# Kernel optimization log

Hardware: AMD Instinct MI355X
Metric: run time of the kernel (lower is better)

Reference implementation:

```python
import jax, jax.numpy as jnp
import numpy as np

B, N, ENC = 128, 196, 2048
DEC, ATT, EMB, V, T = 512, 512, 512, 10000, 21


def setup_inputs() -> dict:
    key = jax.random.key(0)
    ks = jax.random.split(key, 20)
    g = lambda k, shape, scale=0.02: jax.random.normal(k, shape, dtype=jnp.float32) * scale
    return {
        "features": jax.random.normal(ks[0], (B, N, ENC), dtype=jnp.float32),
        "captions": jax.random.randint(ks[1], (B, T), 0, V),
        "emb": g(ks[2], (V, EMB)),
        # attention (weights stored [in, out])
        "U_w": g(ks[3], (ENC, ATT)), "U_b": jnp.zeros((ATT,), jnp.float32),
        "W_w": g(ks[4], (DEC, ATT)), "W_b": jnp.zeros((ATT,), jnp.float32),
        "A_w": g(ks[5], (ATT, 1)),   "A_b": jnp.zeros((1,), jnp.float32),
        # init hidden state
        "ih_w": g(ks[6], (ENC, DEC)), "ih_b": jnp.zeros((DEC,), jnp.float32),
        "ic_w": g(ks[7], (ENC, DEC)), "ic_b": jnp.zeros((DEC,), jnp.float32),
        # LSTMCell, torch gate order (i, f, g, o); stored [in, 4*DEC]
        "lstm_Wih": g(ks[8], (EMB + ENC, 4 * DEC)),
        "lstm_Whh": g(ks[9], (DEC, 4 * DEC)),
        "lstm_bih": jnp.zeros((4 * DEC,), jnp.float32),
        "lstm_bhh": jnp.zeros((4 * DEC,), jnp.float32),
        # output projection
        "fcn_w": g(ks[10], (DEC, V)), "fcn_b": jnp.zeros((V,), jnp.float32),
    }


def reference(features, captions, emb, U_w, U_b, W_w, W_b, A_w, A_b,
              ih_w, ih_b, ic_w, ic_b,
              lstm_Wih, lstm_Whh, lstm_bih, lstm_bhh, fcn_w, fcn_b):
    # init hidden state from mean-pooled features
    mean_feat = features.mean(axis=1)                      # [B, ENC]
    h0 = mean_feat @ ih_w + ih_b                           # [B, DEC]
    c0 = mean_feat @ ic_w + ic_b

    # U(features) is constant across timesteps -> precompute
    u_hs = jnp.einsum('bne,ea->bna', features, U_w) + U_b  # [B, N, ATT]

    embeds = emb[captions[:, :T - 1]]                       # [B, S, EMB]
    embeds_t = jnp.swapaxes(embeds, 0, 1)                   # [S, B, EMB]

    def step(carry, emb_t):
        h, c = carry
        # Bahdanau attention
        w_ah = h @ W_w + W_b                                # [B, ATT]
        scores = (jnp.tanh(u_hs + w_ah[:, None, :]) @ A_w)[..., 0] + A_b[0]  # [B, N]
        alpha = jax.nn.softmax(scores, axis=1)
        context = jnp.einsum('bn,bne->be', alpha, features) # [B, ENC]
        # LSTMCell
        x = jnp.concatenate([emb_t, context], axis=1)       # [B, EMB+ENC]
        gates = x @ lstm_Wih + lstm_bih + h @ lstm_Whh + lstm_bhh
        i, f, g, o = jnp.split(gates, 4, axis=1)
        c = jax.nn.sigmoid(f) * c + jax.nn.sigmoid(i) * jnp.tanh(g)
        h = jax.nn.sigmoid(o) * jnp.tanh(c)
        out = h @ fcn_w + fcn_b                             # [B, V] (dropout = identity in eval)
        return (h, c), (out, alpha)

    (_, _), (preds_t, alphas_t) = jax.lax.scan(step, (h0, c0), embeds_t)
    preds = jnp.swapaxes(preds_t, 0, 1)                     # [B, S, V]
    alphas = jnp.swapaxes(alphas_t, 0, 1)                   # [B, S, N]
    return preds, alphas
```

## Files before the change

### kernel.cpp

```cpp
#include <hip/hip_runtime.h>
#include <cmath>

#define B_   128
#define N_   196
#define ENC_ 2048
#define DEC_ 512
#define ATT_ 512
#define EMB_ 512
#define V_   10000
#define TS_  20
#define HCAT_ 12672
#define HOUT_ 2560

typedef unsigned short u16;
typedef short s16x8 __attribute__((ext_vector_type(8)));
typedef float f32x4 __attribute__((ext_vector_type(4)));
typedef unsigned short u16x4 __attribute__((ext_vector_type(4)));

__device__ __forceinline__ float sigmoidf_(float x) { return 1.0f / (1.0f + expf(-x)); }

__device__ __forceinline__ float fast_tanh(float x) {
  float cx = fminf(fmaxf(x, -8.f), 8.f);
  float e = __expf(2.f * cx);
  return (e - 1.f) * __builtin_amdgcn_rcpf(e + 1.f);
}

__device__ __forceinline__ u16 f2bf(float x) {
  union { float f; unsigned u; } v; v.f = x;
  unsigned r = v.u + 0x7fff + ((v.u >> 16) & 1);
  return (u16)(r >> 16);
}
__device__ __forceinline__ float bf2f(u16 h) {
  union { float f; unsigned u; } v; v.u = ((unsigned)h) << 16; return v.f;
}

typedef const __attribute__((address_space(1))) void gas_t;
typedef __attribute__((address_space(3))) void las_t;
__device__ __forceinline__ void gld_lds16(const void* g, void* l) {
  __builtin_amdgcn_global_load_lds((gas_t*)g, (las_t*)l, 16, 0, 0);
}

__global__ __launch_bounds__(256, 2) void k_mfma(
    const u16* __restrict__ A, int lda,
    const u16* __restrict__ Bt, int ldb,
    const float* __restrict__ bias,
    float* __restrict__ C, u16* __restrict__ Cb, int ldc, int Nbound,
    float* __restrict__ C2, int csplit, int ldc2,
    int K, int atomic) {
  __shared__ __align__(16) u16 As[2][128 * 32];
  __shared__ __align__(16) u16 Bs[2][128 * 32];

  const int tid = threadIdx.x;
  const int bm = blockIdx.y * 128;
  const int bn = blockIdx.x * 128;
  const int kchunk = K / gridDim.z;
  const int k0 = blockIdx.z * kchunk;
  const int kend = k0 + kchunk;

  const int r0 = tid >> 2;
  const int kb = (tid & 3) * 8;
  const u16* ga0 = A + (size_t)(bm + r0) * lda + kb;
  const u16* ga1 = A + (size_t)(bm + 64 + r0) * lda + kb;
  const u16* gb0 = Bt + (size_t)(bn + r0) * ldb + kb;
  const u16* gb1 = Bt + (size_t)(bn + 64 + r0) * ldb + kb;

  const int w = tid >> 6;
  const int lane = tid & 63;
  const int wm = (w & 1) * 64;
  const int wn = (w >> 1) * 64;
  const int r16 = lane & 15;
  const int kq = lane >> 4;

  f32x4 acc[4][4] = {};

  auto STAGE = [&](int buf, int k) {
    gld_lds16(ga0 + k, &As[buf][tid * 8]);
    gld_lds16(ga1 + k, &As[buf][2048 + tid * 8]);
    gld_lds16(gb0 + k, &Bs[buf][tid * 8]);
    gld_lds16(gb1 + k, &Bs[buf][2048 + tid * 8]);
  };

  STAGE(0, k0);
  __syncthreads();
  int cur = 0;
  for (int k = k0; k < kend; k += 32) {
    if (k + 32 < kend) STAGE(cur ^ 1, k + 32);
    s16x8 af[4], bfr[4];
#pragma unroll
    for (int i = 0; i < 4; ++i)
      af[i] = *(const s16x8*)&As[cur][(wm + i * 16 + r16) * 32 + kq * 8];
#pragma unroll
    for (int i = 0; i < 4; ++i)
      bfr[i] = *(const s16x8*)&Bs[cur][(wn + i * 16 + r16) * 32 + kq * 8];
#pragma unroll
    for (int mi = 0; mi < 4; ++mi)
#pragma unroll
      for (int ni = 0; ni < 4; ++ni)
        acc[mi][ni] = __builtin_amdgcn_mfma_f32_16x16x32_bf16(af[mi], bfr[ni], acc[mi][ni], 0, 0, 0);
    __syncthreads();
    cur ^= 1;
  }

#pragma unroll
  for (int ni = 0; ni < 4; ++ni) {
    int col = bn + wn + ni * 16 + r16;
    if (col < Nbound) {
      float bv = bias ? bias[col] : 0.f;
#pragma unroll
      for (int mi = 0; mi < 4; ++mi) {
#pragma unroll
        for (int r = 0; r < 4; ++r) {
          int row = bm + wm + mi * 16 + kq * 4 + r;
          float v = acc[mi][ni][r] + bv;
          if (atomic)                     atomicAdd(&C[(size_t)row * ldc + col], v);
          else if (Cb)                    Cb[(size_t)row * ldc + col] = f2bf(v);
          else if (C2 && col >= csplit)   C2[(size_t)row * ldc2 + (col - csplit)] = v;
          else                            C[(size_t)row * ldc + col] = v;
        }
      }
    }
  }
}

__global__ __launch_bounds__(256) void k_wt(const float* __restrict__ in, int K, int N,
                                            u16* __restrict__ out, int ldo, int Nout) {
  __shared__ float s[32][33];
  int k0 = blockIdx.x * 32, n0 = blockIdx.y * 32;
  int tx = threadIdx.x & 31, ty = threadIdx.x >> 5;
#pragma unroll
  for (int i = 0; i < 4; ++i) {
    int k = k0 + ty + i * 8, n = n0 + tx;
    s[ty + i * 8][tx] = (n < N) ? in[(size_t)k * N + n] : 0.f;
  }
  __syncthreads();
#pragma unroll
  for (int i = 0; i < 4; ++i) {
    int n = n0 + ty + i * 8;
    if (n < Nout) out[(size_t)n * ldo + k0 + tx] = f2bf(s[tx][ty + i * 8]);
  }
}

__global__ __launch_bounds__(256) void k_hbias(const float* __restrict__ W_b,
                                               const float* __restrict__ bih,
                                               const float* __restrict__ bhh,
                                               const float* __restrict__ fcn_b,
                                               float* __restrict__ hbias) {
  int i = blockIdx.x * 256 + threadIdx.x;
  if (i >= HCAT_) return;
  float v;
  if (i < 512)        v = W_b[i];
  else if (i < 2560)  v = bih[i - 512] + bhh[i - 512];
  else if (i < 12560) v = fcn_b[i - 2560];
  else                v = 0.f;
  hbias[i] = v;
}

__global__ __launch_bounds__(256) void k_embed_all(const float* __restrict__ emb,
                                                   const int* __restrict__ captions,
                                                   u16* __restrict__ emb_all_bf) {
  int r = blockIdx.y;
  int t = r >> 7, b = r & 127;
  int k = blockIdx.x * 256 + threadIdx.x;
  int tok = captions[b * 21 + t];
  emb_all_bf[(size_t)r * EMB_ + k] = f2bf(emb[(size_t)tok * EMB_ + k]);
}

__global__ __launch_bounds__(256) void k_cvtmean(const float* __restrict__ f,
                                                 u16* __restrict__ feat_bf,
                                                 u16* __restrict__ mean_bf) {
  int b = blockIdx.y;
  int e = (blockIdx.x * 256 + threadIdx.x) * 4;
  const float* p = f + (size_t)b * N_ * ENC_ + e;
  u16* q = feat_bf + (size_t)b * N_ * ENC_ + e;
  float s0 = 0.f, s1 = 0.f, s2 = 0.f, s3 = 0.f;
#pragma unroll 2
  for (int n = 0; n < N_; ++n) {
    float4 v = *(const float4*)(p + (size_t)n * ENC_);
    s0 += v.x; s1 += v.y; s2 += v.z; s3 += v.w;
    u16x4 o; o.x = f2bf(v.x); o.y = f2bf(v.y); o.z = f2bf(v.z); o.w = f2bf(v.w);
    *(u16x4*)(q + (size_t)n * ENC_) = o;
  }
  const float inv = 1.0f / (float)N_;
  u16x4 m; m.x = f2bf(s0 * inv); m.y = f2bf(s1 * inv);
  m.z = f2bf(s2 * inv); m.w = f2bf(s3 * inv);
  *(u16x4*)(mean_bf + b * ENC_ + e) = m;
}

__global__ __launch_bounds__(256) void k_scores(const u16* __restrict__ u_hs,
                                                const float* __restrict__ w_ah, int ldw,
                                                const float* __restrict__ A_w,
                                                const float* __restrict__ A_b,
                                                float* __restrict__ scores) {
  int wave = threadIdx.x >> 6;
  int lane = threadIdx.x & 63;
  int bn = blockIdx.x * 4 + wave;
  int b = bn / N_;
  int a0 = lane * 8;
  const u16* up = u_hs + (size_t)bn * ATT_ + a0;
  const float* wp = w_ah + (size_t)b * ldw + a0;
  float s = 0.f;
#pragma unroll
  for (int j = 0; j < 2; ++j) {
    u16x4 uv = *(const u16x4*)(up + j * 4);
    float4 wv = *(const float4*)(wp + j * 4);
    float4 aw = *(const float4*)(A_w + a0 + j * 4);
    s += fast_tanh(bf2f(uv.x) + wv.x) * aw.x;
    s += fast_tanh(bf2f(uv.y) + wv.y) * aw.y;
    s += fast_tanh(bf2f(uv.z) + wv.z) * aw.z;
    s += fast_tanh(bf2f(uv.w) + wv.w) * aw.w;
  }
#pragma unroll
  for (int off = 32; off; off >>= 1) s += __shfl_down(s, off);
  if (lane == 0) scores[bn] = s + A_b[0];
}

__global__ __launch_bounds__(256) void k_ctx(const float* __restrict__ scores,
                                             const u16* __restrict__ feat_bf,
                                             const float* __restrict__ embg_t,
                                             const float* __restrict__ houtt,
                                             float* __restrict__ gates,
                                             float* __restrict__ alphas, int t,
                                             u16* __restrict__ ctx_bf) {
  int b = blockIdx.y, tid = threadIdx.x;
  int w = tid >> 6, lane = tid & 63;

  {
    int j0 = blockIdx.x * 1024 + tid * 4;
    float4 eg = *(const float4*)(embg_t + (size_t)b * 2048 + j0);
    float4 hg = *(const float4*)(houtt + (size_t)b * HOUT_ + 512 + j0);
    float4 o; o.x = eg.x + hg.x; o.y = eg.y + hg.y; o.z = eg.z + hg.z; o.w = eg.w + hg.w;
    *(float4*)(gates + (size_t)b * 2048 + j0) = o;
  }

  __shared__ float al[N_];
  __shared__ float wm[4], ws[4];
  __shared__ float bmax, bsum;
  float v = (tid < N_) ? scores[b * N_ + tid] : -1e30f;
  float m = v;
#pragma unroll
  for (int off = 32; off; off >>= 1) m = fmaxf(m, __shfl_down(m, off));
  if (lane == 0) wm[w] = m;
  __syncthreads();
  if (tid == 0) bmax = fmaxf(fmaxf(wm[0], wm[1]), fmaxf(wm[2], wm[3]));
  __syncthreads();
  float e = (tid < N_) ? expf(v - bmax) : 0.f;
  float s = e;
#pragma unroll
  for (int off = 32; off; off >>= 1) s += __shfl_down(s, off);
  if (lane == 0) ws[w] = s;
  __syncthreads();
  if (tid == 0) bsum = ws[0] + ws[1] + ws[2] + ws[3];
  __syncthreads();
  float a = e / bsum;
  if (tid < N_) {
    al[tid] = a;
    if (blockIdx.x == 0) alphas[((size_t)b * TS_ + t) * N_ + tid] = a;
  }
  __syncthreads();

  int e0 = blockIdx.x * 1024 + tid * 4;
  const u16* fp = feat_bf + (size_t)b * N_ * ENC_ + e0;
  float s0 = 0, s1 = 0, s2 = 0, s3 = 0;
#pragma unroll 4
  for (int n = 0; n < N_; ++n) {
    u16x4 vv = *(const u16x4*)(fp + (size_t)n * ENC_);
    float av = al[n];
    s0 += av * bf2f(vv.x); s1 += av * bf2f(vv.y);
    s2 += av * bf2f(vv.z); s3 += av * bf2f(vv.w);
  }
  u16x4 o; o.x = f2bf(s0); o.y = f2bf(s1); o.z = f2bf(s2); o.w = f2bf(s3);
  *(u16x4*)(ctx_bf + (size_t)b * ENC_ + e0) = o;
}

__global__ __launch_bounds__(256) void k_lstm(const float* __restrict__ gates,
                                              float* __restrict__ c,
                                              u16* __restrict__ h_bf) {
  int b = blockIdx.y;
  int j = blockIdx.x * 256 + threadIdx.x;
  const float* g = gates + (size_t)b * 2048;
  float ig = sigmoidf_(g[j]);
  float fg = sigmoidf_(g[512 + j]);
  float gg = tanhf(g[1024 + j]);
  float og = sigmoidf_(g[1536 + j]);
  float cn = fg * c[b * DEC_ + j] + ig * gg;
  c[b * DEC_ + j] = cn;
  h_bf[(size_t)b * DEC_ + j] = f2bf(og * tanhf(cn));
}

extern "C" void kernel_launch(void* const* d_in, const int* in_sizes, int n_in,
                              void* d_out, int out_size, void* d_ws, size_t ws_size,
                              hipStream_t stream) {
  (void)in_sizes; (void)n_in; (void)out_size; (void)ws_size;

  const float* features = (const float*)d_in[0];
  const int*   captions = (const int*)d_in[1];
  const float* emb      = (const float*)d_in[2];
  const float* U_w      = (const float*)d_in[3];
  const float* U_b      = (const float*)d_in[4];
  const float* W_w      = (const float*)d_in[5];
  const float* W_b      = (const float*)d_in[6];
  const float* A_w      = (const float*)d_in[7];
  const float* A_b      = (const float*)d_in[8];
  const float* ih_w     = (const float*)d_in[9];
  const float* ih_b     = (const float*)d_in[10];
  const float* ic_w     = (const float*)d_in[11];
  const float* ic_b     = (const float*)d_in[12];
  const float* Wih      = (const float*)d_in[13];
  const float* Whh      = (const float*)d_in[14];
  const float* bih      = (const float*)d_in[15];
  const float* bhh      = (const float*)d_in[16];
  const float* fcn_w    = (const float*)d_in[17];
  const float* fcn_b    = (const float*)d_in[18];

  float* preds  = (float*)d_out;
  float* alphas = (float*)d_out + (size_t)B_ * TS_ * V_;

  float* p = (float*)d_ws;
  u16*   u_hs      = (u16*)p;    p += (size_t)B_ * N_ * ATT_ / 2;
  u16*   feat_bf   = (u16*)p;    p += (size_t)B_ * N_ * ENC_ / 2;
  u16*   hcatT     = (u16*)p;    p += (size_t)HCAT_ * DEC_ / 2;
  u16*   U_wT      = (u16*)p;    p += (size_t)ATT_ * ENC_ / 2;
  u16*   ih_wT     = (u16*)p;    p += (size_t)DEC_ * ENC_ / 2;
  u16*   ic_wT     = (u16*)p;    p += (size_t)DEC_ * ENC_ / 2;
  u16*   WihEmbT   = (u16*)p;    p += (size_t)2048 * EMB_ / 2;
  u16*   WihCtxT   = (u16*)p;    p += (size_t)2048 * ENC_ / 2;
  u16*   mean_bf   = (u16*)p;    p += (size_t)B_ * ENC_ / 2;
  u16*   emb_all   = (u16*)p;    p += (size_t)TS_ * B_ * EMB_ / 2;
  u16*   h_bf      = (u16*)p;    p += (size_t)B_ * DEC_ / 2;
  u16*   ctx_bf    = (u16*)p;    p += (size_t)B_ * ENC_ / 2;
  float* embgates  = p;          p += (size_t)TS_ * B_ * 2048;
  float* houtt     = p;          p += (size_t)B_ * HOUT_;
  float* cbuf      = p;          p += (size_t)B_ * DEC_;
  float* scores    = p;          p += (size_t)B_ * N_;
  float* gates     = p;          p += (size_t)B_ * 2048;
  float* hbias     = p;          p += HCAT_;

  k_cvtmean<<<dim3(ENC_ / 1024, B_), 256, 0, stream>>>(features, feat_bf, mean_bf);
  k_wt<<<dim3(ENC_ / 32, ATT_ / 32), 256, 0, stream>>>(U_w, ENC_, ATT_, U_wT, ENC_, ATT_);
  k_wt<<<dim3(ENC_ / 32, DEC_ / 32), 256, 0, stream>>>(ih_w, ENC_, DEC_, ih_wT, ENC_, DEC_);
  k_wt<<<dim3(ENC_ / 32, DEC_ / 32), 256, 0, stream>>>(ic_w, ENC_, DEC_, ic_wT, ENC_, DEC_);
  k_wt<<<dim3(DEC_ / 32, ATT_ / 32), 256, 0, stream>>>(W_w, DEC_, ATT_, hcatT, DEC_, ATT_);
  k_wt<<<dim3(DEC_ / 32, 2048 / 32), 256, 0, stream>>>(Whh, DEC_, 2048, hcatT + (size_t)512 * DEC_, DEC_, 2048);
  k_wt<<<dim3(DEC_ / 32, 10112 / 32), 256, 0, stream>>>(fcn_w, DEC_, V_, hcatT + (size_t)2560 * DEC_, DEC_, 10112);
  k_wt<<<dim3(EMB_ / 32, 2048 / 32), 256, 0, stream>>>(Wih, EMB_, 2048, WihEmbT, EMB_, 2048);
  k_wt<<<dim3(ENC_ / 32, 2048 / 32), 256, 0, stream>>>(Wih + (size_t)EMB_ * 2048, ENC_, 2048, WihCtxT, ENC_, 2048);
  k_hbias<<<(HCAT_ + 255) / 256, 256, 0, stream>>>(W_b, bih, bhh, fcn_b, hbias);
  k_embed_all<<<dim3(EMB_ / 256, TS_ * B_), 256, 0, stream>>>(emb, captions, emb_all);

  k_mfma<<<dim3(4, 1, 1), 256, 0, stream>>>(mean_bf, ENC_, ih_wT, ENC_, ih_b,
                                            nullptr, h_bf, DEC_, DEC_, nullptr, 0, 0, ENC_, 0);
  k_mfma<<<dim3(4, 1, 1), 256, 0, stream>>>(mean_bf, ENC_, ic_wT, ENC_, ic_b,
                                            cbuf, nullptr, DEC_, DEC_, nullptr, 0, 0, ENC_, 0);
  k_mfma<<<dim3(ATT_ / 128, (B_ * N_) / 128, 1), 256, 0, stream>>>(
      feat_bf, ENC_, U_wT, ENC_, U_b, nullptr, u_hs, ATT_, ATT_, nullptr, 0, 0, ENC_, 0);
  k_mfma<<<dim3(2048 / 128, TS_, 1), 256, 0, stream>>>(
      emb_all, EMB_, WihEmbT, EMB_, nullptr, embgates, nullptr, 2048, 2048, nullptr, 0, 0, EMB_, 0);

  for (int t = 0; t < TS_; ++t) {
    if (t == 0) {
      k_mfma<<<dim3(HOUT_ / 128, 1, 1), 256, 0, stream>>>(
          h_bf, DEC_, hcatT, DEC_, hbias, houtt, nullptr, HOUT_, HOUT_,
          nullptr, 0, 0, DEC_, 0);
    } else {
      k_mfma<<<dim3(HCAT_ / 128, 1, 1), 256, 0, stream>>>(
          h_bf, DEC_, hcatT, DEC_, hbias, houtt, nullptr, HOUT_, 12560,
          preds + (size_t)(t - 1) * V_, HOUT_, TS_ * V_, DEC_, 0);
    }

    k_scores<<<(B_ * N_) / 4, 256, 0, stream>>>(u_hs, houtt, HOUT_, A_w, A_b, scores);

    k_ctx<<<dim3(2, B_), 256, 0, stream>>>(scores, feat_bf, embgates + (size_t)t * B_ * 2048,
                                           houtt, gates, alphas, t, ctx_bf);

    k_mfma<<<dim3(2048 / 128, 1, 8), 256, 0, stream>>>(
        ctx_bf, ENC_, WihCtxT, ENC_, nullptr, gates, nullptr, 2048, 2048, nullptr, 0, 0, ENC_, 1);

    k_lstm<<<dim3(DEC_ / 256, B_), 256, 0, stream>>>(gates, cbuf, h_bf);
  }

  k_mfma<<<dim3(10112 / 128, 1, 1), 256, 0, stream>>>(
      h_bf, DEC_, hcatT + (size_t)2560 * DEC_, DEC_, hbias + 2560,
      preds + (size_t)(TS_ - 1) * V_, nullptr, TS_ * V_, V_, nullptr, 0, 0, DEC_, 0);
}
```

Baseline: 1.885 ms.

## Replace split-K atomics with partial buffers reduced in LSTM, widen GEMM K-tile

```diff
diff --git a/kernel.cpp b/kernel.cpp
--- a/kernel.cpp
+++ b/kernel.cpp
@@ -11,18 +11,22 @@
 #define TS_  20
 #define HCAT_ 12672
 #define HOUT_ 2560
+#define KSPLIT_ 8
 
 typedef unsigned short u16;
 typedef short s16x8 __attribute__((ext_vector_type(8)));
 typedef float f32x4 __attribute__((ext_vector_type(4)));
 typedef unsigned short u16x4 __attribute__((ext_vector_type(4)));
-
-__device__ __forceinline__ float sigmoidf_(float x) { return 1.0f / (1.0f + expf(-x)); }
+typedef unsigned short u16x2 __attribute__((ext_vector_type(2)));
 
 __device__ __forceinline__ float fast_tanh(float x) {
   float cx = fminf(fmaxf(x, -8.f), 8.f);
   float e = __expf(2.f * cx);
   return (e - 1.f) * __builtin_amdgcn_rcpf(e + 1.f);
+}
+__device__ __forceinline__ float fast_sigmoid(float x) {
+  float cx = fminf(fmaxf(x, -30.f), 30.f);
+  return __builtin_amdgcn_rcpf(1.f + __expf(-cx));
 }
 
 __device__ __forceinline__ u16 f2bf(float x) {
@@ -46,9 +50,9 @@
     const float* __restrict__ bias,
     float* __restrict__ C, u16* __restrict__ Cb, int ldc, int Nbound,
     float* __restrict__ C2, int csplit, int ldc2,
-    int K, int atomic) {
-  __shared__ __align__(16) u16 As[2][128 * 32];
-  __shared__ __align__(16) u16 Bs[2][128 * 32];
+    int K, int mode) {
+  __shared__ __align__(16) u16 As[2][128 * 64];
+  __shared__ __align__(16) u16 Bs[2][128 * 64];
 
   const int tid = threadIdx.x;
   const int bm = blockIdx.y * 128;
@@ -56,13 +60,12 @@
   const int kchunk = K / gridDim.z;
   const int k0 = blockIdx.z * kchunk;
   const int kend = k0 + kchunk;
-
-  const int r0 = tid >> 2;
-  const int kb = (tid & 3) * 8;
-  const u16* ga0 = A + (size_t)(bm + r0) * lda + kb;
-  const u16* ga1 = A + (size_t)(bm + 64 + r0) * lda + kb;
-  const u16* gb0 = Bt + (size_t)(bn + r0) * ldb + kb;
-  const u16* gb1 = Bt + (size_t)(bn + 64 + r0) * ldb + kb;
+  if (mode == 2) C += (size_t)blockIdx.z * 128 * ldc;
+
+  const int r0 = tid >> 3;
+  const int kb = (tid & 7) * 8;
+  const u16* ga = A + (size_t)(bm + r0) * lda + kb;
+  const u16* gb = Bt + (size_t)(bn + r0) * ldb + kb;
 
   const int w = tid >> 6;
   const int lane = tid & 63;
@@ -74,29 +77,33 @@
   f32x4 acc[4][4] = {};
 
   auto STAGE = [&](int buf, int k) {
-    gld_lds16(ga0 + k, &As[buf][tid * 8]);
-    gld_lds16(ga1 + k, &As[buf][2048 + tid * 8]);
-    gld_lds16(gb0 + k, &Bs[buf][tid * 8]);
-    gld_lds16(gb1 + k, &Bs[buf][2048 + tid * 8]);
+#pragma unroll
+    for (int j = 0; j < 4; ++j) {
+      gld_lds16(ga + (size_t)(j * 32) * lda + k, &As[buf][j * 2048 + tid * 8]);
+      gld_lds16(gb + (size_t)(j * 32) * ldb + k, &Bs[buf][j * 2048 + tid * 8]);
+    }
   };
 
   STAGE(0, k0);
   __syncthreads();
   int cur = 0;
-  for (int k = k0; k < kend; k += 32) {
-    if (k + 32 < kend) STAGE(cur ^ 1, k + 32);
-    s16x8 af[4], bfr[4];
-#pragma unroll
-    for (int i = 0; i < 4; ++i)
-      af[i] = *(const s16x8*)&As[cur][(wm + i * 16 + r16) * 32 + kq * 8];
-#pragma unroll
-    for (int i = 0; i < 4; ++i)
-      bfr[i] = *(const s16x8*)&Bs[cur][(wn + i * 16 + r16) * 32 + kq * 8];
-#pragma unroll
-    for (int mi = 0; mi < 4; ++mi)
-#pragma unroll
-      for (int ni = 0; ni < 4; ++ni)
-        acc[mi][ni] = __builtin_amdgcn_mfma_f32_16x16x32_bf16(af[mi], bfr[ni], acc[mi][ni], 0, 0, 0);
+  for (int k = k0; k < kend; k += 64) {
+    if (k + 64 < kend) STAGE(cur ^ 1, k + 64);
+    s16x8 af[2][4], bfr[2][4];
+#pragma unroll
+    for (int s = 0; s < 2; ++s)
+#pragma unroll
+      for (int i = 0; i < 4; ++i) {
+        af[s][i]  = *(const s16x8*)&As[cur][(wm + i * 16 + r16) * 64 + s * 32 + kq * 8];
+        bfr[s][i] = *(const s16x8*)&Bs[cur][(wn + i * 16 + r16) * 64 + s * 32 + kq * 8];
+      }
+#pragma unroll
+    for (int s = 0; s < 2; ++s)
+#pragma unroll
+      for (int mi = 0; mi < 4; ++mi)
+#pragma unroll
+        for (int ni = 0; ni < 4; ++ni)
+          acc[mi][ni] = __builtin_amdgcn_mfma_f32_16x16x32_bf16(af[s][mi], bfr[s][ni], acc[mi][ni], 0, 0, 0);
     __syncthreads();
     cur ^= 1;
   }
@@ -112,7 +119,7 @@
         for (int r = 0; r < 4; ++r) {
           int row = bm + wm + mi * 16 + kq * 4 + r;
           float v = acc[mi][ni][r] + bv;
-          if (atomic)                     atomicAdd(&C[(size_t)row * ldc + col], v);
+          if (mode == 1)                  atomicAdd(&C[(size_t)row * ldc + col], v);
           else if (Cb)                    Cb[(size_t)row * ldc + col] = f2bf(v);
           else if (C2 && col >= csplit)   C2[(size_t)row * ldc2 + (col - csplit)] = v;
           else                            C[(size_t)row * ldc + col] = v;
@@ -214,26 +221,15 @@
   if (lane == 0) scores[bn] = s + A_b[0];
 }
 
-__global__ __launch_bounds__(256) void k_ctx(const float* __restrict__ scores,
+__global__ __launch_bounds__(512) void k_ctx(const float* __restrict__ scores,
                                              const u16* __restrict__ feat_bf,
-                                             const float* __restrict__ embg_t,
-                                             const float* __restrict__ houtt,
-                                             float* __restrict__ gates,
                                              float* __restrict__ alphas, int t,
                                              u16* __restrict__ ctx_bf) {
   int b = blockIdx.y, tid = threadIdx.x;
   int w = tid >> 6, lane = tid & 63;
 
-  {
-    int j0 = blockIdx.x * 1024 + tid * 4;
-    float4 eg = *(const float4*)(embg_t + (size_t)b * 2048 + j0);
-    float4 hg = *(const float4*)(houtt + (size_t)b * HOUT_ + 512 + j0);
-    float4 o; o.x = eg.x + hg.x; o.y = eg.y + hg.y; o.z = eg.z + hg.z; o.w = eg.w + hg.w;
-    *(float4*)(gates + (size_t)b * 2048 + j0) = o;
-  }
-
   __shared__ float al[N_];
-  __shared__ float wm[4], ws[4];
+  __shared__ float wm[8], ws[8];
   __shared__ float bmax, bsum;
   float v = (tid < N_) ? scores[b * N_ + tid] : -1e30f;
   float m = v;
@@ -241,15 +237,25 @@
   for (int off = 32; off; off >>= 1) m = fmaxf(m, __shfl_down(m, off));
   if (lane == 0) wm[w] = m;
   __syncthreads();
-  if (tid == 0) bmax = fmaxf(fmaxf(wm[0], wm[1]), fmaxf(wm[2], wm[3]));
-  __syncthreads();
-  float e = (tid < N_) ? expf(v - bmax) : 0.f;
+  if (tid == 0) {
+    float bm0 = wm[0];
+#pragma unroll
+    for (int i = 1; i < 8; ++i) bm0 = fmaxf(bm0, wm[i]);
+    bmax = bm0;
+  }
+  __syncthreads();
+  float e = (tid < N_) ? __expf(v - bmax) : 0.f;
   float s = e;
 #pragma unroll
   for (int off = 32; off; off >>= 1) s += __shfl_down(s, off);
   if (lane == 0) ws[w] = s;
   __syncthreads();
-  if (tid == 0) bsum = ws[0] + ws[1] + ws[2] + ws[3];
+  if (tid == 0) {
+    float bs0 = 0.f;
+#pragma unroll
+    for (int i = 0; i < 8; ++i) bs0 += ws[i];
+    bsum = bs0;
+  }
   __syncthreads();
   float a = e / bsum;
   if (tid < N_) {
@@ -258,33 +264,43 @@
   }
   __syncthreads();
 
-  int e0 = blockIdx.x * 1024 + tid * 4;
+  int e0 = blockIdx.x * 1024 + tid * 2;
   const u16* fp = feat_bf + (size_t)b * N_ * ENC_ + e0;
-  float s0 = 0, s1 = 0, s2 = 0, s3 = 0;
-#pragma unroll 4
+  float s0 = 0, s1 = 0;
+#pragma unroll 8
   for (int n = 0; n < N_; ++n) {
-    u16x4 vv = *(const u16x4*)(fp + (size_t)n * ENC_);
+    u16x2 vv = *(const u16x2*)(fp + (size_t)n * ENC_);
     float av = al[n];
     s0 += av * bf2f(vv.x); s1 += av * bf2f(vv.y);
-    s2 += av * bf2f(vv.z); s3 += av * bf2f(vv.w);
-  }
-  u16x4 o; o.x = f2bf(s0); o.y = f2bf(s1); o.z = f2bf(s2); o.w = f2bf(s3);
-  *(u16x4*)(ctx_bf + (size_t)b * ENC_ + e0) = o;
-}
-
-__global__ __launch_bounds__(256) void k_lstm(const float* __restrict__ gates,
+  }
+  u16x2 o; o.x = f2bf(s0); o.y = f2bf(s1);
+  *(u16x2*)(ctx_bf + (size_t)b * ENC_ + e0) = o;
+}
+
+__global__ __launch_bounds__(256) void k_lstm(const float* __restrict__ gatesP,
+                                              const float* __restrict__ embg_t,
+                                              const float* __restrict__ houtt,
                                               float* __restrict__ c,
                                               u16* __restrict__ h_bf) {
   int b = blockIdx.y;
   int j = blockIdx.x * 256 + threadIdx.x;
-  const float* g = gates + (size_t)b * 2048;
-  float ig = sigmoidf_(g[j]);
-  float fg = sigmoidf_(g[512 + j]);
-  float gg = tanhf(g[1024 + j]);
-  float og = sigmoidf_(g[1536 + j]);
+  float g4[4];
+#pragma unroll
+  for (int gi = 0; gi < 4; ++gi) {
+    int col = gi * 512 + j;
+    float s = embg_t[(size_t)b * 2048 + col] + houtt[(size_t)b * HOUT_ + 512 + col];
+#pragma unroll
+    for (int z = 0; z < KSPLIT_; ++z)
+      s += gatesP[(size_t)z * B_ * 2048 + (size_t)b * 2048 + col];
+    g4[gi] = s;
+  }
+  float ig = fast_sigmoid(g4[0]);
+  float fg = fast_sigmoid(g4[1]);
+  float gg = fast_tanh(g4[2]);
+  float og = fast_sigmoid(g4[3]);
   float cn = fg * c[b * DEC_ + j] + ig * gg;
   c[b * DEC_ + j] = cn;
-  h_bf[(size_t)b * DEC_ + j] = f2bf(og * tanhf(cn));
+  h_bf[(size_t)b * DEC_ + j] = f2bf(og * fast_tanh(cn));
 }
 
 extern "C" void kernel_launch(void* const* d_in, const int* in_sizes, int n_in,
@@ -332,7 +348,7 @@
   float* houtt     = p;          p += (size_t)B_ * HOUT_;
   float* cbuf      = p;          p += (size_t)B_ * DEC_;
   float* scores    = p;          p += (size_t)B_ * N_;
-  float* gates     = p;          p += (size_t)B_ * 2048;
+  float* gatesP    = p;          p += (size_t)KSPLIT_ * B_ * 2048;
   float* hbias     = p;          p += HCAT_;
 
   k_cvtmean<<<dim3(ENC_ / 1024, B_), 256, 0, stream>>>(features, feat_bf, mean_bf);
@@ -369,13 +385,13 @@
 
     k_scores<<<(B_ * N_) / 4, 256, 0, stream>>>(u_hs, houtt, HOUT_, A_w, A_b, scores);
 
-    k_ctx<<<dim3(2, B_), 256, 0, stream>>>(scores, feat_bf, embgates + (size_t)t * B_ * 2048,
-                                           houtt, gates, alphas, t, ctx_bf);
-
-    k_mfma<<<dim3(2048 / 128, 1, 8), 256, 0, stream>>>(
-        ctx_bf, ENC_, WihCtxT, ENC_, nullptr, gates, nullptr, 2048, 2048, nullptr, 0, 0, ENC_, 1);
-
-    k_lstm<<<dim3(DEC_ / 256, B_), 256, 0, stream>>>(gates, cbuf, h_bf);
+    k_ctx<<<dim3(2, B_), 512, 0, stream>>>(scores, feat_bf, alphas, t, ctx_bf);
+
+    k_mfma<<<dim3(2048 / 128, 1, KSPLIT_), 256, 0, stream>>>(
+        ctx_bf, ENC_, WihCtxT, ENC_, nullptr, gatesP, nullptr, 2048, 2048, nullptr, 0, 0, ENC_, 2);
+
+    k_lstm<<<dim3(DEC_ / 256, B_), 256, 0, stream>>>(gatesP, embgates + (size_t)t * B_ * 2048,
+                                                     houtt, cbuf, h_bf);
   }
 
   k_mfma<<<dim3(10112 / 128, 1, 1), 256, 0, stream>>>(
```

Result: slower. 1.974 ms (+4.7%).
